# Kernel optimization log

Hardware: AMD Instinct MI355X
Metric: run time of the kernel (lower is better)

The kernel has to match this reference:

```python
import jax, jax.numpy as jnp
import numpy as np

B, H, W, C = 32, 112, 112, 96
NH, WS, SHIFT = 3, 7, 3
HID = 4 * C
N = WS * WS
HD = C // NH


def setup_inputs() -> dict:
    key = jax.random.key(0)
    ks = jax.random.split(key, 8)
    s = 0.02
    inp = {}
    inp['x'] = jax.random.normal(ks[0], (B, H * W, C), jnp.float32)
    # --- standard Swin shift attention mask ---
    img = np.zeros((1, H, W, 1), np.float32)
    cnt = 0
    for hs in (slice(0, -WS), slice(-WS, -SHIFT), slice(-SHIFT, None)):
        for wsl in (slice(0, -WS), slice(-WS, -SHIFT), slice(-SHIFT, None)):
            img[:, hs, wsl, :] = cnt
            cnt += 1
    mw = img.reshape(1, H // WS, WS, W // WS, WS, 1).transpose(0, 1, 3, 2, 4, 5).reshape(-1, N)
    am = mw[:, None, :] - mw[:, :, None]
    inp['attn_mask'] = jnp.asarray(np.where(am != 0, -100.0, 0.0).astype(np.float32))
    # --- relative position index ---
    coords = np.stack(np.meshgrid(np.arange(WS), np.arange(WS), indexing='ij'))  # (2, ws, ws)
    cf = coords.reshape(2, -1)
    rel = (cf[:, :, None] - cf[:, None, :]).transpose(1, 2, 0)  # (N, N, 2)
    rel[:, :, 0] += WS - 1
    rel[:, :, 1] += WS - 1
    rel[:, :, 0] *= 2 * WS - 1
    inp['rel_index'] = jnp.asarray(rel.sum(-1).astype(np.int32))  # (N, N)
    # --- params ---
    inp['norm1_g'] = jnp.ones((C,), jnp.float32)
    inp['norm1_b'] = jnp.zeros((C,), jnp.float32)
    inp['qkv_w'] = jax.random.normal(ks[1], (3 * C, C), jnp.float32) * s
    inp['qkv_b'] = jnp.zeros((3 * C,), jnp.float32)
    inp['proj_w'] = jax.random.normal(ks[2], (C, C), jnp.float32) * s
    inp['proj_b'] = jnp.zeros((C,), jnp.float32)
    inp['rel_bias_table'] = jax.random.normal(ks[3], ((2 * WS - 1) ** 2, NH), jnp.float32) * s
    inp['norm2_g'] = jnp.ones((C,), jnp.float32)
    inp['norm2_b'] = jnp.zeros((C,), jnp.float32)
    inp['fc1_w'] = jax.random.normal(ks[4], (HID, C), jnp.float32) * s
    inp['fc1_b'] = jnp.zeros((HID,), jnp.float32)
    inp['fc2_w'] = jax.random.normal(ks[5], (C, HID), jnp.float32) * s
    inp['fc2_b'] = jnp.zeros((C,), jnp.float32)
    return inp


def _ln(x, g, b):
    m = x.mean(-1, keepdims=True)
    v = ((x - m) ** 2).mean(-1, keepdims=True)
    return (x - m) * jax.lax.rsqrt(v + 1e-5) * g + b


def reference(x, attn_mask, rel_index, norm1_g, norm1_b, qkv_w, qkv_b, proj_w, proj_b,
              rel_bias_table, norm2_g, norm2_b, fc1_w, fc1_b, fc2_w, fc2_b):
    b = x.shape[0]
    shortcut = x
    h = _ln(x, norm1_g, norm1_b).reshape(b, H, W, C)
    # H, W divisible by WS -> pad is a no-op; cyclic shift
    h = jnp.roll(h, (-SHIFT, -SHIFT), axis=(1, 2))
    nWh, nWw = H // WS, W // WS
    nW = nWh * nWw
    # window partition -> (b*nW, N, C)
    xw = h.reshape(b, nWh, WS, nWw, WS, C).transpose(0, 1, 3, 2, 4, 5).reshape(-1, N, C)
    qkv = (xw @ qkv_w.T + qkv_b).reshape(-1, N, 3, NH, HD).transpose(2, 0, 3, 1, 4)
    q, k, v = qkv[0], qkv[1], qkv[2]  # each (b*nW, NH, N, HD)
    q = q * (HD ** -0.5)
    attn = jnp.einsum('whnd,whmd->whnm', q, k)  # (b*nW, NH, N, N)
    bias = rel_bias_table[rel_index.reshape(-1)].reshape(N, N, NH).transpose(2, 0, 1)
    attn = attn + bias[None]
    attn = attn.reshape(b, nW, NH, N, N) + attn_mask[None, :, None]
    attn = jax.nn.softmax(attn, axis=-1).reshape(-1, NH, N, N)
    out = jnp.einsum('whnm,whmd->whnd', attn, v).transpose(0, 2, 1, 3).reshape(-1, N, C)
    out = out @ proj_w.T + proj_b
    # window reverse + reverse shift
    out = out.reshape(b, nWh, nWw, WS, WS, C).transpose(0, 1, 3, 2, 4, 5).reshape(b, H, W, C)
    out = jnp.roll(out, (SHIFT, SHIFT), axis=(1, 2)).reshape(b, H * W, C)
    x1 = shortcut + out
    y = _ln(x1, norm2_g, norm2_b)
    y = jax.nn.gelu(y @ fc1_w.T + fc1_b, approximate=False) @ fc2_w.T + fc2_b
    return x1 + y
```

## Files before the change

kernel.cpp:

```cpp
#include <hip/hip_runtime.h>
#include <hip/hip_bf16.h>
#include <math.h>

#define HH 112
#define WW_ 112
#define CC 96
#define NHH 3
#define WSZ 7
#define SHIFT_ 3
#define NTOK 49
#define HDIM 32
#define WTOT 8192
#define MTOT 401408

typedef __hip_bfloat16 bf16;
typedef __attribute__((ext_vector_type(8))) short short8;
typedef __attribute__((ext_vector_type(4))) float floatx4;

static __device__ __forceinline__ float bits2f(short s) {
  return __uint_as_float(((unsigned)(unsigned short)s) << 16);
}
static __device__ __forceinline__ short f2bits(float v) {
  bf16 h = __float2bfloat16(v);
  short s;
  __builtin_memcpy(&s, &h, 2);
  return s;
}
static __device__ __forceinline__ float bf2f(bf16 v) { return __bfloat162float(v); }
static __device__ __forceinline__ bf16 f2bf(float v) { return __float2bfloat16(v); }

template <typename T> struct IO;
template <> struct IO<float> {
  static __device__ __forceinline__ float ld(const float* p, long i) { return p[i]; }
  static __device__ __forceinline__ void st(float* p, long i, float v) { p[i] = v; }
  static __device__ __forceinline__ short8 frag(const float* p) {
    short8 r;
#pragma unroll
    for (int j = 0; j < 8; ++j) r[j] = f2bits(p[j]);
    return r;
  }
};
template <> struct IO<bf16> {
  static __device__ __forceinline__ float ld(const bf16* p, long i) { return bf2f(p[i]); }
  static __device__ __forceinline__ void st(bf16* p, long i, float v) { p[i] = f2bf(v); }
  static __device__ __forceinline__ short8 frag(const bf16* p) { return *(const short8*)p; }
};

__global__ void detect_kernel(const unsigned short* __restrict__ x, int* flag) {
  __shared__ int tot;
  if (threadIdx.x == 0) tot = 0;
  __syncthreads();
  int bad = 0;
  for (int i = threadIdx.x; i < 8192; i += 256) {
    int e = (x[i] >> 7) & 0xFF;
    if (e >= 0x86) bad++;
  }
  atomicAdd(&tot, bad);
  __syncthreads();
  if (threadIdx.x == 0) *flag = (tot > 64) ? 1 : 0;
}

template <typename T>
__device__ __forceinline__ void combine_body(const T* mask, const int* rel,
                                             const T* bt, bf16* comb) {
  long idx = (long)blockIdx.x * 256 + threadIdx.x;
  long rem = idx % 7203;
  long wi = idx / 7203;
  int h = (int)(rem / 2401);
  int n2 = (int)(rem % 2401);
  float v = IO<T>::ld(bt, (long)rel[n2] * NHH + h) + IO<T>::ld(mask, wi * 2401 + n2);
  comb[idx] = f2bf(v);
}
__global__ __launch_bounds__(256) void combine_kernel(
    const int* __restrict__ flag, const void* mask, const int* __restrict__ rel,
    const void* bt, bf16* __restrict__ comb) {
  if (*flag)
    combine_body<float>((const float*)mask, rel, (const float*)bt, comb);
  else
    combine_body<bf16>((const bf16*)mask, rel, (const bf16*)bt, comb);
}

template <typename T>
__device__ __forceinline__ void qkv_attn_body(
    const T* x, const T* g1, const T* b1, const T* qkv_w, const T* qkv_b,
    const bf16* comb, bf16* attn_out, short* qk, short* R, short* wc,
    float* bq) {
  int win = blockIdx.x;
  int wave = threadIdx.x >> 6;
  int lane = threadIdx.x & 63;
  int col = lane & 15, kg = lane >> 4;
  float* gb = (float*)wc;
  for (int i = threadIdx.x; i < 288; i += 256) bq[i] = IO<T>::ld(qkv_b, i);
  for (int i = threadIdx.x; i < CC; i += 256) {
    gb[i] = IO<T>::ld(g1, i);
    gb[CC + i] = IO<T>::ld(b1, i);
  }
  __syncthreads();
  {
    int r = lane >> 2;
    int seg = lane & 3;
    int n = wave * 16 + r;
    short* dst = R + n * 104 + seg * 24;
    if (n < NTOK) {
      int bq_ = win >> 8, wi = win & 255;
      int wh = wi >> 4, ww = wi & 15;
      int i = n / WSZ, j = n - (n / WSZ) * WSZ;
      int hs = wh * WSZ + i + SHIFT_; if (hs >= HH) hs -= HH;
      int ws = ww * WSZ + j + SHIFT_; if (ws >= WW_) ws -= WW_;
      const T* src = x + ((long)bq_ * (HH * WW_) + (long)hs * WW_ + ws) * CC + seg * 24;
      float a[24];
#pragma unroll
      for (int t = 0; t < 24; ++t) a[t] = IO<T>::ld(src, t);
      float s = 0.f;
#pragma unroll
      for (int t = 0; t < 24; ++t) s += a[t];
      s += __shfl_xor(s, 1, 64);
      s += __shfl_xor(s, 2, 64);
      float mean = s * (1.f / CC);
      float var = 0.f;
#pragma unroll
      for (int t = 0; t < 24; ++t) { float d = a[t] - mean; var += d * d; }
      var += __shfl_xor(var, 1, 64);
      var += __shfl_xor(var, 2, 64);
      float rstd = rsqrtf(var * (1.f / CC) + 1e-5f);
#pragma unroll
      for (int t = 0; t < 24; ++t)
        dst[t] = f2bits((a[t] - mean) * rstd * gb[seg * 24 + t] + gb[CC + seg * 24 + t]);
    } else {
#pragma unroll
      for (int t = 0; t < 24; ++t) dst[t] = 0;
    }
  }
  __syncthreads();
  short8 af[3];
#pragma unroll
  for (int kc = 0; kc < 3; ++kc)
    af[kc] = *(const short8*)(R + (wave * 16 + col) * 104 + kc * 32 + kg * 8);
  const float scale = 0.17677669529663687f;
  for (int c = 0; c < 6; ++c) {
    __syncthreads();
    for (int idx = threadIdx.x; idx < 576; idx += 256) {
      int r = idx / 12, c8 = idx % 12;
      *(short8*)(wc + r * 104 + c8 * 8) =
          IO<T>::frag(qkv_w + (long)(c * 48 + r) * CC + c8 * 8);
    }
    __syncthreads();
#pragma unroll
    for (int t = 0; t < 3; ++t) {
      floatx4 acc = {0.f, 0.f, 0.f, 0.f};
#pragma unroll
      for (int kc = 0; kc < 3; ++kc) {
        short8 bfr = *(const short8*)(wc + (t * 16 + col) * 104 + kc * 32 + kg * 8);
        acc = __builtin_amdgcn_mfma_f32_16x16x32_bf16(af[kc], bfr, acc, 0, 0, 0);
      }
      int nc = c * 3 + t;
      int cc = nc * 16 + col;
      float bb = bq[cc];
      if (nc < 6) {
#pragma unroll
        for (int r = 0; r < 4; ++r)
          qk[(wave * 16 + kg * 4 + r) * 200 + cc] = f2bits((acc[r] + bb) * scale);
      } else if (nc < 12) {
#pragma unroll
        for (int r = 0; r < 4; ++r)
          qk[(wave * 16 + kg * 4 + r) * 200 + cc] = f2bits(acc[r] + bb);
      } else {
        int d = cc - 2 * CC;
#pragma unroll
        for (int r = 0; r < 4; ++r)
          R[d * 68 + wave * 16 + kg * 4 + r] = f2bits(acc[r] + bb);
      }
    }
  }
  __syncthreads();
  floatx4 st[3][4];
#pragma unroll
  for (int h = 0; h < NHH; ++h) {
    short8 qa = *(const short8*)(qk + (wave * 16 + col) * 200 + h * HDIM + kg * 8);
#pragma unroll
    for (int nt = 0; nt < 4; ++nt) {
      short8 kb = *(const short8*)(qk + (nt * 16 + col) * 200 + CC + h * HDIM + kg * 8);
      floatx4 z = {0.f, 0.f, 0.f, 0.f};
      st[h][nt] = __builtin_amdgcn_mfma_f32_16x16x32_bf16(qa, kb, z, 0, 0, 0);
    }
  }
  __syncthreads();
  const bf16* cb = comb + (long)(win & 255) * (NHH * 2401);
#pragma unroll
  for (int h = 0; h < NHH; ++h) {
#pragma unroll
    for (int r = 0; r < 4; ++r) {
      int m = wave * 16 + kg * 4 + r;
      int mc = (m < NTOK) ? m : (NTOK - 1);
      float sv[4];
      float mx = -1e30f;
#pragma unroll
      for (int nt = 0; nt < 4; ++nt) {
        int n = nt * 16 + col;
        float v = (n < NTOK)
                      ? (st[h][nt][r] + bf2f(cb[h * 2401 + mc * NTOK + n]))
                      : -1e30f;
        sv[nt] = v;
        mx = fmaxf(mx, v);
      }
#pragma unroll
      for (int msk = 1; msk < 16; msk <<= 1) mx = fmaxf(mx, __shfl_xor(mx, msk, 64));
      float sum = 0.f;
#pragma unroll
      for (int nt = 0; nt < 4; ++nt) {
        float e = __expf(sv[nt] - mx);
        sv[nt] = e;
        sum += e;
      }
#pragma unroll
      for (int msk = 1; msk < 16; msk <<= 1) sum += __shfl_xor(sum, msk, 64);
      float inv = 1.f / sum;
#pragma unroll
      for (int nt = 0; nt < 4; ++nt)
        qk[m * 200 + h * 64 + nt * 16 + col] = f2bits(sv[nt] * inv);
    }
  }
  __syncthreads();
#pragma unroll
  for (int h = 0; h < NHH; ++h) {
    floatx4 oa[2];
    oa[0] = (floatx4){0.f, 0.f, 0.f, 0.f};
    oa[1] = (floatx4){0.f, 0.f, 0.f, 0.f};
#pragma unroll
    for (int kc = 0; kc < 2; ++kc) {
      short8 pa = *(const short8*)(qk + (wave * 16 + col) * 200 + h * 64 + kc * 32 + kg * 8);
#pragma unroll
      for (int dt = 0; dt < 2; ++dt) {
        short8 vb = *(const short8*)(R + (h * HDIM + dt * 16 + col) * 68 + kc * 32 + kg * 8);
        oa[dt] = __builtin_amdgcn_mfma_f32_16x16x32_bf16(pa, vb, oa[dt], 0, 0, 0);
      }
    }
#pragma unroll
    for (int dt = 0; dt < 2; ++dt)
#pragma unroll
      for (int r = 0; r < 4; ++r) {
        int m = wave * 16 + kg * 4 + r;
        if (m < NTOK)
          attn_out[((long)win * NTOK + m) * CC + h * HDIM + dt * 16 + col] =
              f2bf(oa[dt][r]);
      }
  }
}
__global__ __launch_bounds__(256) void qkv_attn_kernel(
    const int* __restrict__ flag, const void* x, const void* g1, const void* b1,
    const void* qkv_w, const void* qkv_b, const bf16* __restrict__ comb,
    bf16* __restrict__ attn_out) {
  __shared__ short qk[64 * 200];
  __shared__ short R[6656];
  __shared__ short wc[48 * 104];
  __shared__ float bq[288];
  if (*flag)
    qkv_attn_body<float>((const float*)x, (const float*)g1, (const float*)b1,
                         (const float*)qkv_w, (const float*)qkv_b, comb,
                         attn_out, qk, R, wc, bq);
  else
    qkv_attn_body<bf16>((const bf16*)x, (const bf16*)g1, (const bf16*)b1,
                        (const bf16*)qkv_w, (const bf16*)qkv_b, comb, attn_out,
                        qk, R, wc, bq);
}

static __device__ __forceinline__ long scatter_index(long m) {
  int win = (int)(m / NTOK);
  int n = (int)(m - (long)win * NTOK);
  int bq = win >> 8, wi = win & 255;
  int wh = wi >> 4, ww = wi & 15;
  int i = n / WSZ, j = n - (n / WSZ) * WSZ;
  int hf = wh * WSZ + i + SHIFT_; if (hf >= HH) hf -= HH;
  int wf = ww * WSZ + j + SHIFT_; if (wf >= WW_) wf -= WW_;
  return ((long)bq * (HH * WW_) + (long)hf * WW_ + wf) * CC;
}

template <typename T>
__device__ __forceinline__ void proj_body(const bf16* A, const T* W,
                                          const T* bias, T* out, const T* res,
                                          short* wl, float* bl) {
  for (int idx = threadIdx.x; idx < 1152; idx += 256) {
    int r = idx / 12, c8 = idx % 12;
    *(short8*)(wl + r * 104 + c8 * 8) = IO<T>::frag(W + (long)r * CC + c8 * 8);
  }
  for (int i = threadIdx.x; i < CC; i += 256) bl[i] = IO<T>::ld(bias, i);
  __syncthreads();
  int wave = threadIdx.x >> 6;
  int lane = threadIdx.x & 63;
  int col = lane & 15;
  int kg = lane >> 4;
  long mbase = (long)blockIdx.x * 128 + wave * 32;
  short8 a0[3], a1[3];
#pragma unroll
  for (int kc = 0; kc < 3; ++kc) {
    a0[kc] = *(const short8*)(A + (mbase + col) * CC + kc * 32 + kg * 8);
    a1[kc] = *(const short8*)(A + (mbase + 16 + col) * CC + kc * 32 + kg * 8);
  }
  long dst0[4], dst1[4];
#pragma unroll
  for (int r = 0; r < 4; ++r) {
    dst0[r] = scatter_index(mbase + kg * 4 + r);
    dst1[r] = scatter_index(mbase + 16 + kg * 4 + r);
  }
#pragma unroll
  for (int nc = 0; nc < 6; ++nc) {
    floatx4 acc0 = {0.f, 0.f, 0.f, 0.f};
    floatx4 acc1 = {0.f, 0.f, 0.f, 0.f};
#pragma unroll
    for (int kc = 0; kc < 3; ++kc) {
      short8 bfr = *(const short8*)(wl + (nc * 16 + col) * 104 + kc * 32 + kg * 8);
      acc0 = __builtin_amdgcn_mfma_f32_16x16x32_bf16(a0[kc], bfr, acc0, 0, 0, 0);
      acc1 = __builtin_amdgcn_mfma_f32_16x16x32_bf16(a1[kc], bfr, acc1, 0, 0, 0);
    }
    int cc = nc * 16 + col;
    float bb = bl[cc];
#pragma unroll
    for (int r = 0; r < 4; ++r) {
      long p0 = dst0[r] + cc;
      long p1 = dst1[r] + cc;
      IO<T>::st(out, p0, acc0[r] + bb + IO<T>::ld(res, p0));
      IO<T>::st(out, p1, acc1[r] + bb + IO<T>::ld(res, p1));
    }
  }
}
__global__ __launch_bounds__(256) void proj_kernel(
    const int* __restrict__ flag, const bf16* __restrict__ A, const void* W,
    const void* bias, void* out, const void* res) {
  __shared__ short wl[96 * 104];
  __shared__ float bl[CC];
  if (*flag)
    proj_body<float>(A, (const float*)W, (const float*)bias, (float*)out,
                     (const float*)res, wl, bl);
  else
    proj_body<bf16>(A, (const bf16*)W, (const bf16*)bias, (bf16*)out,
                    (const bf16*)res, wl, bl);
}

template <typename T>
__device__ __forceinline__ void mlp_body(const T* n2g, const T* n2b,
                                         const T* fc1_w, const T* fc1_b,
                                         const T* fc2_w, const T* fc2_b, T* xo,
                                         short* xln, short* w1c, short* w2c) {
  int wave = threadIdx.x >> 6;
  int lane = threadIdx.x & 63;
  int col = lane & 15;
  int kg = lane >> 4;
  long mbase = (long)blockIdx.x * 64;
  float* gb = (float*)w2c;
  for (int i = threadIdx.x; i < CC; i += 256) {
    gb[i] = IO<T>::ld(n2g, i);
    gb[CC + i] = IO<T>::ld(n2b, i);
  }
  __syncthreads();
  {
    int r = lane >> 2;
    int seg = lane & 3;
    const T* src = xo + (mbase + wave * 16 + r) * CC + seg * 24;
    float a[24];
#pragma unroll
    for (int t = 0; t < 24; ++t) a[t] = IO<T>::ld(src, t);
    float s = 0.f;
#pragma unroll
    for (int t = 0; t < 24; ++t) s += a[t];
    s += __shfl_xor(s, 1, 64);
    s += __shfl_xor(s, 2, 64);
    float mean = s * (1.f / CC);
    float var = 0.f;
#pragma unroll
    for (int t = 0; t < 24; ++t) { float d = a[t] - mean; var += d * d; }
    var += __shfl_xor(var, 1, 64);
    var += __shfl_xor(var, 2, 64);
    float rstd = rsqrtf(var * (1.f / CC) + 1e-5f);
    short* dst = xln + (wave * 16 + r) * 104 + seg * 24;
#pragma unroll
    for (int t = 0; t < 24; ++t)
      dst[t] = f2bits((a[t] - mean) * rstd * gb[seg * 24 + t] + gb[CC + seg * 24 + t]);
  }
  __syncthreads();
  short8 af[3];
#pragma unroll
  for (int kc = 0; kc < 3; ++kc)
    af[kc] = *(const short8*)(xln + (wave * 16 + col) * 104 + kc * 32 + kg * 8);
  short* h1c = xln;
  floatx4 acc2[6];
#pragma unroll
  for (int i = 0; i < 6; ++i) acc2[i] = (floatx4){0.f, 0.f, 0.f, 0.f};
  for (int c = 0; c < 6; ++c) {
    __syncthreads();
    for (int idx = threadIdx.x; idx < 768; idx += 256) {
      int r = idx / 12, c8 = idx % 12;
      *(short8*)(w1c + r * 104 + c8 * 8) =
          IO<T>::frag(fc1_w + (long)(c * 64 + r) * CC + c8 * 8);
    }
    for (int idx = threadIdx.x; idx < 768; idx += 256) {
      int r = idx / 8, c8 = idx % 8;
      *(short8*)(w2c + r * 72 + c8 * 8) =
          IO<T>::frag(fc2_w + (long)r * 384 + c * 64 + c8 * 8);
    }
    __syncthreads();
#pragma unroll
    for (int t = 0; t < 4; ++t) {
      floatx4 acc = {0.f, 0.f, 0.f, 0.f};
#pragma unroll
      for (int kc = 0; kc < 3; ++kc) {
        short8 bfr = *(const short8*)(w1c + (t * 16 + col) * 104 + kc * 32 + kg * 8);
        acc = __builtin_amdgcn_mfma_f32_16x16x32_bf16(af[kc], bfr, acc, 0, 0, 0);
      }
      float bb = IO<T>::ld(fc1_b, c * 64 + t * 16 + col);
#pragma unroll
      for (int r = 0; r < 4; ++r) {
        float v = acc[r] + bb;
        float ge = 0.5f * v * (1.f + erff(v * 0.70710678118654752f));
        h1c[(wave * 16 + kg * 4 + r) * 72 + t * 16 + col] = f2bits(ge);
      }
    }
    __syncthreads();
    short8 a2[2];
#pragma unroll
    for (int kk = 0; kk < 2; ++kk)
      a2[kk] = *(const short8*)(h1c + (wave * 16 + col) * 72 + kk * 32 + kg * 8);
#pragma unroll
    for (int nc2 = 0; nc2 < 6; ++nc2) {
#pragma unroll
      for (int kk = 0; kk < 2; ++kk) {
        short8 b2f = *(const short8*)(w2c + (nc2 * 16 + col) * 72 + kk * 32 + kg * 8);
        acc2[nc2] = __builtin_amdgcn_mfma_f32_16x16x32_bf16(a2[kk], b2f, acc2[nc2], 0, 0, 0);
      }
    }
  }
#pragma unroll
  for (int nc2 = 0; nc2 < 6; ++nc2) {
    int cc = nc2 * 16 + col;
    float bb = IO<T>::ld(fc2_b, cc);
#pragma unroll
    for (int r = 0; r < 4; ++r) {
      long p = (mbase + wave * 16 + kg * 4 + r) * CC + cc;
      IO<T>::st(xo, p, acc2[nc2][r] + bb + IO<T>::ld(xo, p));
    }
  }
}
__global__ __launch_bounds__(256) void mlp_kernel(
    const int* __restrict__ flag, const void* n2g, const void* n2b,
    const void* fc1_w, const void* fc1_b, const void* fc2_w, const void* fc2_b,
    void* xo) {
  __shared__ short xln[64 * 104];
  __shared__ short w1c[64 * 104];
  __shared__ short w2c[96 * 72];
  if (*flag)
    mlp_body<float>((const float*)n2g, (const float*)n2b, (const float*)fc1_w,
                    (const float*)fc1_b, (const float*)fc2_w,
                    (const float*)fc2_b, (float*)xo, xln, w1c, w2c);
  else
    mlp_body<bf16>((const bf16*)n2g, (const bf16*)n2b, (const bf16*)fc1_w,
                   (const bf16*)fc1_b, (const bf16*)fc2_w, (const bf16*)fc2_b,
                   (bf16*)xo, xln, w1c, w2c);
}

extern "C" void kernel_launch(void* const* d_in, const int* in_sizes, int n_in,
                              void* d_out, int out_size, void* d_ws, size_t ws_size,
                              hipStream_t stream) {
  (void)in_sizes; (void)n_in; (void)out_size; (void)ws_size;
  char* ws = (char*)d_ws;
  bf16* bufA = (bf16*)ws;
  size_t offA = (size_t)MTOT * CC * 2;
  bf16* comb = (bf16*)(ws + offA);
  size_t offC = offA + (size_t)256 * NHH * 2401 * 2;
  int* flag = (int*)(ws + offC);

  const int* rel_index = (const int*)d_in[2];

  detect_kernel<<<1, 256, 0, stream>>>((const unsigned short*)d_in[0], flag);
  combine_kernel<<<7203, 256, 0, stream>>>(flag, d_in[1], rel_index, d_in[9], comb);
  qkv_attn_kernel<<<WTOT, 256, 0, stream>>>(flag, d_in[0], d_in[3], d_in[4],
                                            d_in[5], d_in[6], comb, bufA);
  proj_kernel<<<MTOT / 128, 256, 0, stream>>>(flag, bufA, d_in[7], d_in[8],
                                              d_out, d_in[0]);
  mlp_kernel<<<MTOT / 64, 256, 0, stream>>>(flag, d_in[10], d_in[11], d_in[12],
                                            d_in[13], d_in[14], d_in[15], d_out);
}
```

Baseline: 813.6 us.

## Load MFMA weight fragments directly from global and drop LDS weight staging

In the QKV/attention, projection and MLP kernels, weight tiles are no longer copied into shared memory. Each wave now reads its MFMA B fragments straight from global memory through the caches, which removes many block-wide barriers and per-chunk staging loops. Barriers that only guarded per-wave rows are also dropped. LDS row strides are padded to 204 and 76 to avoid bank conflicts, and launch bounds are raised to ask for 4 blocks per CU. The cost is that every wave re-fetches and converts the full weight set, which adds cache and global traffic and repeated fp32-to-bf16 conversion.

```diff
diff --git a/kernel.cpp b/kernel.cpp
--- a/kernel.cpp
+++ b/kernel.cpp
@@ -12,6 +12,8 @@
 #define HDIM 32
 #define WTOT 8192
 #define MTOT 401408
+#define QKS 204
+#define H1S 76
 
 typedef __hip_bfloat16 bf16;
 typedef __attribute__((ext_vector_type(8))) short short8;
@@ -83,14 +85,11 @@
 template <typename T>
 __device__ __forceinline__ void qkv_attn_body(
     const T* x, const T* g1, const T* b1, const T* qkv_w, const T* qkv_b,
-    const bf16* comb, bf16* attn_out, short* qk, short* R, short* wc,
-    float* bq) {
+    const bf16* comb, bf16* attn_out, short* qk, short* R, float* gb) {
   int win = blockIdx.x;
   int wave = threadIdx.x >> 6;
   int lane = threadIdx.x & 63;
   int col = lane & 15, kg = lane >> 4;
-  float* gb = (float*)wc;
-  for (int i = threadIdx.x; i < 288; i += 256) bq[i] = IO<T>::ld(qkv_b, i);
   for (int i = threadIdx.x; i < CC; i += 256) {
     gb[i] = IO<T>::ld(g1, i);
     gb[CC + i] = IO<T>::ld(b1, i);
@@ -131,55 +130,50 @@
       for (int t = 0; t < 24; ++t) dst[t] = 0;
     }
   }
-  __syncthreads();
   short8 af[3];
 #pragma unroll
   for (int kc = 0; kc < 3; ++kc)
     af[kc] = *(const short8*)(R + (wave * 16 + col) * 104 + kc * 32 + kg * 8);
   const float scale = 0.17677669529663687f;
-  for (int c = 0; c < 6; ++c) {
-    __syncthreads();
-    for (int idx = threadIdx.x; idx < 576; idx += 256) {
-      int r = idx / 12, c8 = idx % 12;
-      *(short8*)(wc + r * 104 + c8 * 8) =
-          IO<T>::frag(qkv_w + (long)(c * 48 + r) * CC + c8 * 8);
-    }
-    __syncthreads();
-#pragma unroll
-    for (int t = 0; t < 3; ++t) {
-      floatx4 acc = {0.f, 0.f, 0.f, 0.f};
-#pragma unroll
-      for (int kc = 0; kc < 3; ++kc) {
-        short8 bfr = *(const short8*)(wc + (t * 16 + col) * 104 + kc * 32 + kg * 8);
-        acc = __builtin_amdgcn_mfma_f32_16x16x32_bf16(af[kc], bfr, acc, 0, 0, 0);
-      }
-      int nc = c * 3 + t;
-      int cc = nc * 16 + col;
-      float bb = bq[cc];
-      if (nc < 6) {
-#pragma unroll
-        for (int r = 0; r < 4; ++r)
-          qk[(wave * 16 + kg * 4 + r) * 200 + cc] = f2bits((acc[r] + bb) * scale);
-      } else if (nc < 12) {
-#pragma unroll
-        for (int r = 0; r < 4; ++r)
-          qk[(wave * 16 + kg * 4 + r) * 200 + cc] = f2bits(acc[r] + bb);
-      } else {
-        int d = cc - 2 * CC;
-#pragma unroll
-        for (int r = 0; r < 4; ++r)
-          R[d * 68 + wave * 16 + kg * 4 + r] = f2bits(acc[r] + bb);
-      }
-    }
+#pragma unroll
+  for (int nc = 0; nc < 12; ++nc) {
+    floatx4 acc = {0.f, 0.f, 0.f, 0.f};
+#pragma unroll
+    for (int kc = 0; kc < 3; ++kc) {
+      short8 bfr = IO<T>::frag(qkv_w + (long)(nc * 16 + col) * CC + kc * 32 + kg * 8);
+      acc = __builtin_amdgcn_mfma_f32_16x16x32_bf16(af[kc], bfr, acc, 0, 0, 0);
+    }
+    int cc = nc * 16 + col;
+    float bb = IO<T>::ld(qkv_b, cc);
+    float m = (nc < 6) ? scale : 1.f;
+#pragma unroll
+    for (int r = 0; r < 4; ++r)
+      qk[(wave * 16 + kg * 4 + r) * QKS + cc] = f2bits((acc[r] + bb) * m);
+  }
+  __syncthreads();
+#pragma unroll
+  for (int nc = 12; nc < 18; ++nc) {
+    floatx4 acc = {0.f, 0.f, 0.f, 0.f};
+#pragma unroll
+    for (int kc = 0; kc < 3; ++kc) {
+      short8 bfr = IO<T>::frag(qkv_w + (long)(nc * 16 + col) * CC + kc * 32 + kg * 8);
+      acc = __builtin_amdgcn_mfma_f32_16x16x32_bf16(af[kc], bfr, acc, 0, 0, 0);
+    }
+    int cc = nc * 16 + col;
+    float bb = IO<T>::ld(qkv_b, cc);
+    int d = cc - 2 * CC;
+#pragma unroll
+    for (int r = 0; r < 4; ++r)
+      R[d * 68 + wave * 16 + kg * 4 + r] = f2bits(acc[r] + bb);
   }
   __syncthreads();
   floatx4 st[3][4];
 #pragma unroll
   for (int h = 0; h < NHH; ++h) {
-    short8 qa = *(const short8*)(qk + (wave * 16 + col) * 200 + h * HDIM + kg * 8);
+    short8 qa = *(const short8*)(qk + (wave * 16 + col) * QKS + h * HDIM + kg * 8);
 #pragma unroll
     for (int nt = 0; nt < 4; ++nt) {
-      short8 kb = *(const short8*)(qk + (nt * 16 + col) * 200 + CC + h * HDIM + kg * 8);
+      short8 kb = *(const short8*)(qk + (nt * 16 + col) * QKS + CC + h * HDIM + kg * 8);
       floatx4 z = {0.f, 0.f, 0.f, 0.f};
       st[h][nt] = __builtin_amdgcn_mfma_f32_16x16x32_bf16(qa, kb, z, 0, 0, 0);
     }
@@ -217,10 +211,9 @@
       float inv = 1.f / sum;
 #pragma unroll
       for (int nt = 0; nt < 4; ++nt)
-        qk[m * 200 + h * 64 + nt * 16 + col] = f2bits(sv[nt] * inv);
-    }
-  }
-  __syncthreads();
+        qk[m * QKS + h * 64 + nt * 16 + col] = f2bits(sv[nt] * inv);
+    }
+  }
 #pragma unroll
   for (int h = 0; h < NHH; ++h) {
     floatx4 oa[2];
@@ -228,7 +221,7 @@
     oa[1] = (floatx4){0.f, 0.f, 0.f, 0.f};
 #pragma unroll
     for (int kc = 0; kc < 2; ++kc) {
-      short8 pa = *(const short8*)(qk + (wave * 16 + col) * 200 + h * 64 + kc * 32 + kg * 8);
+      short8 pa = *(const short8*)(qk + (wave * 16 + col) * QKS + h * 64 + kc * 32 + kg * 8);
 #pragma unroll
       for (int dt = 0; dt < 2; ++dt) {
         short8 vb = *(const short8*)(R + (h * HDIM + dt * 16 + col) * 68 + kc * 32 + kg * 8);
@@ -246,22 +239,21 @@
       }
   }
 }
-__global__ __launch_bounds__(256) void qkv_attn_kernel(
+__global__ __launch_bounds__(256, 4) void qkv_attn_kernel(
     const int* __restrict__ flag, const void* x, const void* g1, const void* b1,
     const void* qkv_w, const void* qkv_b, const bf16* __restrict__ comb,
     bf16* __restrict__ attn_out) {
-  __shared__ short qk[64 * 200];
+  __shared__ short qk[64 * QKS];
   __shared__ short R[6656];
-  __shared__ short wc[48 * 104];
-  __shared__ float bq[288];
+  __shared__ float gb[192];
   if (*flag)
     qkv_attn_body<float>((const float*)x, (const float*)g1, (const float*)b1,
                          (const float*)qkv_w, (const float*)qkv_b, comb,
-                         attn_out, qk, R, wc, bq);
+                         attn_out, qk, R, gb);
   else
     qkv_attn_body<bf16>((const bf16*)x, (const bf16*)g1, (const bf16*)b1,
                         (const bf16*)qkv_w, (const bf16*)qkv_b, comb, attn_out,
-                        qk, R, wc, bq);
+                        qk, R, gb);
 }
 
 static __device__ __forceinline__ long scatter_index(long m) {
@@ -277,14 +269,7 @@
 
 template <typename T>
 __device__ __forceinline__ void proj_body(const bf16* A, const T* W,
-                                          const T* bias, T* out, const T* res,
-                                          short* wl, float* bl) {
-  for (int idx = threadIdx.x; idx < 1152; idx += 256) {
-    int r = idx / 12, c8 = idx % 12;
-    *(short8*)(wl + r * 104 + c8 * 8) = IO<T>::frag(W + (long)r * CC + c8 * 8);
-  }
-  for (int i = threadIdx.x; i < CC; i += 256) bl[i] = IO<T>::ld(bias, i);
-  __syncthreads();
+                                          const T* bias, T* out, const T* res) {
   int wave = threadIdx.x >> 6;
   int lane = threadIdx.x & 63;
   int col = lane & 15;
@@ -308,12 +293,12 @@
     floatx4 acc1 = {0.f, 0.f, 0.f, 0.f};
 #pragma unroll
     for (int kc = 0; kc < 3; ++kc) {
-      short8 bfr = *(const short8*)(wl + (nc * 16 + col) * 104 + kc * 32 + kg * 8);
+      short8 bfr = IO<T>::frag(W + (long)(nc * 16 + col) * CC + kc * 32 + kg * 8);
       acc0 = __builtin_amdgcn_mfma_f32_16x16x32_bf16(a0[kc], bfr, acc0, 0, 0, 0);
       acc1 = __builtin_amdgcn_mfma_f32_16x16x32_bf16(a1[kc], bfr, acc1, 0, 0, 0);
     }
     int cc = nc * 16 + col;
-    float bb = bl[cc];
+    float bb = IO<T>::ld(bias, cc);
 #pragma unroll
     for (int r = 0; r < 4; ++r) {
       long p0 = dst0[r] + cc;
@@ -323,30 +308,27 @@
     }
   }
 }
-__global__ __launch_bounds__(256) void proj_kernel(
+__global__ __launch_bounds__(256, 4) void proj_kernel(
     const int* __restrict__ flag, const bf16* __restrict__ A, const void* W,
     const void* bias, void* out, const void* res) {
-  __shared__ short wl[96 * 104];
-  __shared__ float bl[CC];
   if (*flag)
     proj_body<float>(A, (const float*)W, (const float*)bias, (float*)out,
-                     (const float*)res, wl, bl);
+                     (const float*)res);
   else
     proj_body<bf16>(A, (const bf16*)W, (const bf16*)bias, (bf16*)out,
-                    (const bf16*)res, wl, bl);
+                    (const bf16*)res);
 }
 
 template <typename T>
 __device__ __forceinline__ void mlp_body(const T* n2g, const T* n2b,
                                          const T* fc1_w, const T* fc1_b,
                                          const T* fc2_w, const T* fc2_b, T* xo,
-                                         short* xln, short* w1c, short* w2c) {
+                                         short* xln, short* h1c, float* gb) {
   int wave = threadIdx.x >> 6;
   int lane = threadIdx.x & 63;
   int col = lane & 15;
   int kg = lane >> 4;
   long mbase = (long)blockIdx.x * 64;
-  float* gb = (float*)w2c;
   for (int i = threadIdx.x; i < CC; i += 256) {
     gb[i] = IO<T>::ld(n2g, i);
     gb[CC + i] = IO<T>::ld(n2b, i);
@@ -376,34 +358,21 @@
     for (int t = 0; t < 24; ++t)
       dst[t] = f2bits((a[t] - mean) * rstd * gb[seg * 24 + t] + gb[CC + seg * 24 + t]);
   }
-  __syncthreads();
   short8 af[3];
 #pragma unroll
   for (int kc = 0; kc < 3; ++kc)
     af[kc] = *(const short8*)(xln + (wave * 16 + col) * 104 + kc * 32 + kg * 8);
-  short* h1c = xln;
   floatx4 acc2[6];
 #pragma unroll
   for (int i = 0; i < 6; ++i) acc2[i] = (floatx4){0.f, 0.f, 0.f, 0.f};
   for (int c = 0; c < 6; ++c) {
-    __syncthreads();
-    for (int idx = threadIdx.x; idx < 768; idx += 256) {
-      int r = idx / 12, c8 = idx % 12;
-      *(short8*)(w1c + r * 104 + c8 * 8) =
-          IO<T>::frag(fc1_w + (long)(c * 64 + r) * CC + c8 * 8);
-    }
-    for (int idx = threadIdx.x; idx < 768; idx += 256) {
-      int r = idx / 8, c8 = idx % 8;
-      *(short8*)(w2c + r * 72 + c8 * 8) =
-          IO<T>::frag(fc2_w + (long)r * 384 + c * 64 + c8 * 8);
-    }
-    __syncthreads();
 #pragma unroll
     for (int t = 0; t < 4; ++t) {
       floatx4 acc = {0.f, 0.f, 0.f, 0.f};
 #pragma unroll
       for (int kc = 0; kc < 3; ++kc) {
-        short8 bfr = *(const short8*)(w1c + (t * 16 + col) * 104 + kc * 32 + kg * 8);
+        short8 bfr =
+            IO<T>::frag(fc1_w + (long)(c * 64 + t * 16 + col) * CC + kc * 32 + kg * 8);
         acc = __builtin_amdgcn_mfma_f32_16x16x32_bf16(af[kc], bfr, acc, 0, 0, 0);
       }
       float bb = IO<T>::ld(fc1_b, c * 64 + t * 16 + col);
@@ -411,19 +380,19 @@
       for (int r = 0; r < 4; ++r) {
         float v = acc[r] + bb;
         float ge = 0.5f * v * (1.f + erff(v * 0.70710678118654752f));
-        h1c[(wave * 16 + kg * 4 + r) * 72 + t * 16 + col] = f2bits(ge);
-      }
-    }
-    __syncthreads();
+        h1c[(wave * 16 + kg * 4 + r) * H1S + t * 16 + col] = f2bits(ge);
+      }
+    }
     short8 a2[2];
 #pragma unroll
     for (int kk = 0; kk < 2; ++kk)
-      a2[kk] = *(const short8*)(h1c + (wave * 16 + col) * 72 + kk * 32 + kg * 8);
+      a2[kk] = *(const short8*)(h1c + (wave * 16 + col) * H1S + kk * 32 + kg * 8);
 #pragma unroll
     for (int nc2 = 0; nc2 < 6; ++nc2) {
 #pragma unroll
       for (int kk = 0; kk < 2; ++kk) {
-        short8 b2f = *(const short8*)(w2c + (nc2 * 16 + col) * 72 + kk * 32 + kg * 8);
+        short8 b2f = IO<T>::frag(fc2_w + (long)(nc2 * 16 + col) * (4 * CC) + c * 64 +
+                                 kk * 32 + kg * 8);
         acc2[nc2] = __builtin_amdgcn_mfma_f32_16x16x32_bf16(a2[kk], b2f, acc2[nc2], 0, 0, 0);
       }
     }
@@ -439,21 +408,21 @@
     }
   }
 }
-__global__ __launch_bounds__(256) void mlp_kernel(
+__global__ __launch_bounds__(256, 4) void mlp_kernel(
     const int* __restrict__ flag, const void* n2g, const void* n2b,
     const void* fc1_w, const void* fc1_b, const void* fc2_w, const void* fc2_b,
     void* xo) {
   __shared__ short xln[64 * 104];
-  __shared__ short w1c[64 * 104];
-  __shared__ short w2c[96 * 72];
+  __shared__ short h1c[64 * H1S];
+  __shared__ float gb[192];
   if (*flag)
     mlp_body<float>((const float*)n2g, (const float*)n2b, (const float*)fc1_w,
                     (const float*)fc1_b, (const float*)fc2_w,
-                    (const float*)fc2_b, (float*)xo, xln, w1c, w2c);
+                    (const float*)fc2_b, (float*)xo, xln, h1c, gb);
   else
     mlp_body<bf16>((const bf16*)n2g, (const bf16*)n2b, (const bf16*)fc1_w,
                    (const bf16*)fc1_b, (const bf16*)fc2_w, (const bf16*)fc2_b,
-                   (bf16*)xo, xln, w1c, w2c);
+                   (bf16*)xo, xln, h1c, gb);
 }
 
 extern "C" void kernel_launch(void* const* d_in, const int* in_sizes, int n_in,
```

Result: slower. 1.636 ms (+101.0%).
